# Kernel optimization log

Measured on AMD Instinct MI355X. Metric: run time of the kernel, lower is better.

## Reference

```python
import jax, jax.numpy as jnp
import numpy as np

B, F, T, C = 2, 4, 1024, 1536   # batch, features, ticks, channels
NW = [476, 476, 292]            # wires per plane (same layout for both faces)
NX = 1536                       # wire crossings per face


def _make_wc(rng, nw, nchan):
    # rows: (wire_ident, channel); idents form a permutation of [0, nw)
    ident = rng.permutation(nw)
    chan = rng.integers(0, nchan, size=nw)
    return jnp.asarray(np.stack([ident, chan], axis=1), dtype=jnp.int32)


def setup_inputs() -> dict:
    key = jax.random.key(0)
    rng = np.random.default_rng(0)
    x = jax.random.normal(key, (B, F, T, C), dtype=jnp.float32)
    wcs = {f"wc{i}{j}": _make_wc(rng, NW[j], C) for i in range(2) for j in range(3)}
    xms = {f"xm{i}": jnp.asarray(
        np.stack([rng.integers(0, NW[j], size=NX) for j in range(3)], axis=1),
        dtype=jnp.int32) for i in range(2)}
    w_seg = jax.random.normal(jax.random.fold_in(key, 1), (1, F), dtype=jnp.float32) * 0.1
    b_seg = jnp.zeros((1,), dtype=jnp.float32)
    return {"x": x, **wcs, **xms, "w_seg": w_seg, "b_seg": b_seg}


def _face(x, wcs_face, xm):
    # x: (B,F,T,C); wcs_face: list of 3 (nw,2) int maps; xm: (NX,3)
    outs = []
    for j in range(3):
        ident, chan = wcs_face[j][:, 0], wcs_face[j][:, 1]
        nw = wcs_face[j].shape[0]
        # gather channels, reindex into wire order (scatter-set by wire ident)
        wsv = jnp.zeros(x.shape[:-1] + (nw,), x.dtype).at[..., ident].set(x[..., chan])
        idx = xm[:, j]                                  # (NX,)
        gathered = wsv[..., idx]                        # (B,F,T,NX); crossover term == identity
        # segment-mean back onto wires: scatter_add + count + clamp(min=1)
        summed = jnp.zeros_like(wsv).at[..., idx].add(gathered)
        cnt = jnp.zeros((nw,), x.dtype).at[idx].add(1.0)
        summed = summed / jnp.clip(cnt, 1.0, None)
        outs.append((summed, chan))
    return outs


def reference(x, wc00, wc01, wc02, wc10, wc11, wc12, xm0, xm1, w_seg, b_seg):
    wcs = [[wc00, wc01, wc02], [wc10, wc11, wc12]]
    xms = [xm0, xm1]
    nchan = x.shape[-1]
    y = jnp.zeros_like(x)                # (B,F,T,C)
    cy = jnp.zeros((nchan,), x.dtype)
    for i in range(2):
        for summed, chan in _face(x, wcs[i], xms[i]):
            y = y.at[..., chan].add(summed)   # scatter-add wire terms onto channels
            cy = cy.at[chan].add(1.0)
    y = y / jnp.clip(cy, 1.0, None)
    y = jnp.transpose(y, (0, 1, 3, 2))        # (B,F,C,T)
    logits = jnp.einsum('bfct,of->boct', y, w_seg) + b_seg[None, :, None, None]
    return jax.nn.sigmoid(logits)             # (B,1,C,T)
```

## Files before the change

### kernel.cpp

```cpp
#include <hip/hip_runtime.h>

#define B_ 2
#define F_ 4
#define T_ 1024
#define C_ 1536
#define NX_ 1536
#define CAP 64

__global__ __launch_bounds__(1024) void build_meta(
    const int* __restrict__ wc00, const int* __restrict__ wc01, const int* __restrict__ wc02,
    const int* __restrict__ wc10, const int* __restrict__ wc11, const int* __restrict__ wc12,
    const int* __restrict__ xm0, const int* __restrict__ xm1,
    int nw0, int nw1, int nw2,
    int* __restrict__ masks,
    int* __restrict__ cyInt,
    int* __restrict__ count,
    int* __restrict__ edges,
    float* __restrict__ scale)
{
    const int tid = threadIdx.x;
    const int nth = blockDim.x;
    const int* wcs[6] = {wc00, wc01, wc02, wc10, wc11, wc12};
    const int* xms[2] = {xm0, xm1};
    int nws[3] = {nw0, nw1, nw2};
    int moff[6];
    int tot = 0;
    for (int f = 0; f < 6; ++f) { moff[f] = tot; tot += nws[f % 3]; }

    for (int s = tid; s < tot; s += nth) masks[s] = 0;
    for (int c = tid; c < C_; c += nth) { cyInt[c] = 0; count[c] = 0; }
    __syncthreads();

    for (int i = 0; i < 2; ++i)
        for (int j = 0; j < 3; ++j) {
            const int f = i * 3 + j;
            const int* xm = xms[i];
            for (int p = tid; p < NX_; p += nth) {
                int s = xm[p * 3 + j];
                masks[moff[f] + s] = 1;
            }
        }
    for (int f = 0; f < 6; ++f) {
        const int nw = nws[f % 3];
        const int* wc = wcs[f];
        for (int s = tid; s < nw; s += nth) atomicAdd(&cyInt[wc[s * 2 + 1]], 1);
    }
    __syncthreads();

    for (int f = 0; f < 6; ++f) {
        const int nw = nws[f % 3];
        const int* wc = wcs[f];
        for (int k = tid; k < nw; k += nth) {
            int s = wc[k * 2 + 0];
            if (masks[moff[f] + s]) {
                int dst = wc[s * 2 + 1];
                int src = wc[k * 2 + 1];
                int pos = atomicAdd(&count[dst], 1);
                if (pos < CAP) edges[dst * CAP + pos] = src;
            }
        }
    }
    __syncthreads();

    for (int c = tid; c < C_; c += nth) {
        int cv = cyInt[c];
        scale[c] = 1.0f / (float)(cv > 0 ? cv : 1);
    }
}

#define TILE 64
__global__ __launch_bounds__(256) void zT_kernel(
    const float* __restrict__ x, const float* __restrict__ w_seg,
    float* __restrict__ zT)
{
    __shared__ float tile[TILE][TILE + 1];
    const int b  = blockIdx.z;
    const int t0 = blockIdx.x * TILE;
    const int c0 = blockIdx.y * TILE;
    const int tx = threadIdx.x & 63;
    const int ty = threadIdx.x >> 6;

    const float w0 = w_seg[0], w1 = w_seg[1], w2 = w_seg[2], w3 = w_seg[3];
    const float* xb = x + (size_t)b * F_ * T_ * C_;
    const size_t fstride = (size_t)T_ * C_;

    for (int tt = ty; tt < TILE; tt += 4) {
        const size_t base = (size_t)(t0 + tt) * C_ + c0 + tx;
        float acc = w0 * xb[base]
                  + w1 * xb[base + fstride]
                  + w2 * xb[base + 2 * fstride]
                  + w3 * xb[base + 3 * fstride];
        tile[tt][tx] = acc;
    }
    __syncthreads();

    float* zb = zT + (size_t)b * C_ * T_;
    for (int cc = ty; cc < TILE; cc += 4) {
        zb[(size_t)(c0 + cc) * T_ + t0 + tx] = tile[tx][cc];
    }
}

__global__ __launch_bounds__(256) void gather_out(
    const float* __restrict__ zT,
    const int* __restrict__ edges, const int* __restrict__ count,
    const float* __restrict__ scale, const float* __restrict__ b_seg,
    float* __restrict__ out)
{
    const int c = blockIdx.x;
    const int b = blockIdx.y;
    const int n = min(count[c], CAP);
    const float sc = scale[c];
    const float bs = b_seg[0];

    const float* zb = zT + (size_t)b * C_ * T_;
    const int t = threadIdx.x * 4;

    float4 acc = make_float4(0.f, 0.f, 0.f, 0.f);
    for (int e = 0; e < n; ++e) {
        const int src = edges[c * CAP + e];
        const float4 v = *reinterpret_cast<const float4*>(zb + (size_t)src * T_ + t);
        acc.x += v.x; acc.y += v.y; acc.z += v.z; acc.w += v.w;
    }
    float4 o;
    o.x = 1.f / (1.f + expf(-(acc.x * sc + bs)));
    o.y = 1.f / (1.f + expf(-(acc.y * sc + bs)));
    o.z = 1.f / (1.f + expf(-(acc.z * sc + bs)));
    o.w = 1.f / (1.f + expf(-(acc.w * sc + bs)));
    *reinterpret_cast<float4*>(out + ((size_t)b * C_ + c) * T_ + t) = o;
}

extern "C" void kernel_launch(void* const* d_in, const int* in_sizes, int n_in,
                              void* d_out, int out_size, void* d_ws, size_t ws_size,
                              hipStream_t stream) {
    const float* x     = (const float*)d_in[0];
    const int* wc00    = (const int*)d_in[1];
    const int* wc01    = (const int*)d_in[2];
    const int* wc02    = (const int*)d_in[3];
    const int* wc10    = (const int*)d_in[4];
    const int* wc11    = (const int*)d_in[5];
    const int* wc12    = (const int*)d_in[6];
    const int* xm0     = (const int*)d_in[7];
    const int* xm1     = (const int*)d_in[8];
    const float* w_seg = (const float*)d_in[9];
    const float* b_seg = (const float*)d_in[10];
    float* out         = (float*)d_out;

    const int nw0 = in_sizes[1] / 2;
    const int nw1 = in_sizes[2] / 2;
    const int nw2 = in_sizes[3] / 2;

    char* ws = (char*)d_ws;
    size_t off = 0;
    float* zT   = (float*)(ws + off); off += (size_t)B_ * C_ * T_ * sizeof(float);
    int* edges  = (int*)(ws + off);   off += (size_t)C_ * CAP * sizeof(int);
    int* count  = (int*)(ws + off);   off += (size_t)C_ * sizeof(int);
    int* cyInt  = (int*)(ws + off);   off += (size_t)C_ * sizeof(int);
    float* scale= (float*)(ws + off); off += (size_t)C_ * sizeof(float);
    int* masks  = (int*)(ws + off);   off += (size_t)2 * (nw0 + nw1 + nw2) * sizeof(int);

    build_meta<<<1, 1024, 0, stream>>>(wc00, wc01, wc02, wc10, wc11, wc12,
                                       xm0, xm1, nw0, nw1, nw2,
                                       masks, cyInt, count, edges, scale);

    zT_kernel<<<dim3(T_ / TILE, C_ / TILE, B_), 256, 0, stream>>>(x, w_seg, zT);

    gather_out<<<dim3(C_, B_), 256, 0, stream>>>(zT, edges, count, scale, b_seg, out);
}
```

Before: 128.4 us.

## Fuse metadata build into transpose kernel as extra block with shared-memory atomics

Merges the single-block metadata construction into the weighted-transpose kernel as one extra block, so its work overlaps with the transpose instead of running as a separate serial launch. The metadata masks, counts and channel tallies now live in shared memory instead of global memory. The transpose loads and stores are widened to float4. The cost is a larger shared-memory union (about 28KB) per block, which may reduce occupancy of the transpose blocks, and a hardcoded 4096-entry mask array.

Result: faster. 120.7 us (-6.0%).

```diff
diff --git a/kernel.cpp b/kernel.cpp
--- a/kernel.cpp
+++ b/kernel.cpp
@@ -6,97 +6,119 @@
 #define C_ 1536
 #define NX_ 1536
 #define CAP 64
+#define TILE 64
+#define ZT_BLOCKS ((T_ / TILE) * (C_ / TILE) * B_)
 
-__global__ __launch_bounds__(1024) void build_meta(
+struct MetaSh {
+    int masks[4096];
+    int cnt[C_];
+    int cy[C_];
+};
+
+union SharedU {
+    float tile[TILE][TILE + 1];
+    MetaSh m;
+};
+
+__global__ __launch_bounds__(256) void zt_meta(
+    const float* __restrict__ x, const float* __restrict__ w_seg,
+    float* __restrict__ zT,
     const int* __restrict__ wc00, const int* __restrict__ wc01, const int* __restrict__ wc02,
     const int* __restrict__ wc10, const int* __restrict__ wc11, const int* __restrict__ wc12,
     const int* __restrict__ xm0, const int* __restrict__ xm1,
     int nw0, int nw1, int nw2,
-    int* __restrict__ masks,
-    int* __restrict__ cyInt,
     int* __restrict__ count,
     int* __restrict__ edges,
     float* __restrict__ scale)
 {
+    __shared__ SharedU sh;
     const int tid = threadIdx.x;
-    const int nth = blockDim.x;
-    const int* wcs[6] = {wc00, wc01, wc02, wc10, wc11, wc12};
-    const int* xms[2] = {xm0, xm1};
-    int nws[3] = {nw0, nw1, nw2};
-    int moff[6];
-    int tot = 0;
-    for (int f = 0; f < 6; ++f) { moff[f] = tot; tot += nws[f % 3]; }
 
-    for (int s = tid; s < tot; s += nth) masks[s] = 0;
-    for (int c = tid; c < C_; c += nth) { cyInt[c] = 0; count[c] = 0; }
-    __syncthreads();
+    if (blockIdx.x == ZT_BLOCKS) {
+        const int* wcs[6] = {wc00, wc01, wc02, wc10, wc11, wc12};
+        const int* xms[2] = {xm0, xm1};
+        int nws[3] = {nw0, nw1, nw2};
+        int moff[6];
+        int tot = 0;
+        for (int f = 0; f < 6; ++f) { moff[f] = tot; tot += nws[f % 3]; }
 
-    for (int i = 0; i < 2; ++i)
-        for (int j = 0; j < 3; ++j) {
-            const int f = i * 3 + j;
-            const int* xm = xms[i];
-            for (int p = tid; p < NX_; p += nth) {
-                int s = xm[p * 3 + j];
-                masks[moff[f] + s] = 1;
+        for (int s = tid; s < 4096; s += 256) sh.m.masks[s] = 0;
+        for (int c = tid; c < C_; c += 256) { sh.m.cnt[c] = 0; sh.m.cy[c] = 0; }
+        __syncthreads();
+
+        for (int i = 0; i < 2; ++i)
+            for (int j = 0; j < 3; ++j) {
+                const int f = i * 3 + j;
+                const int* xm = xms[i];
+                for (int p = tid; p < NX_; p += 256)
+                    sh.m.masks[moff[f] + xm[p * 3 + j]] = 1;
+            }
+        __syncthreads();
+
+        for (int f = 0; f < 6; ++f) {
+            const int nw = nws[f % 3];
+            const int* wc = wcs[f];
+            for (int k = tid; k < nw; k += 256) {
+                const int src = wc[k * 2 + 1];
+                atomicAdd(&sh.m.cy[src], 1);
+                const int s = wc[k * 2 + 0];
+                if (sh.m.masks[moff[f] + s]) {
+                    const int dst = wc[s * 2 + 1];
+                    const int pos = atomicAdd(&sh.m.cnt[dst], 1);
+                    if (pos < CAP) edges[dst * CAP + pos] = src;
+                }
             }
         }
-    for (int f = 0; f < 6; ++f) {
-        const int nw = nws[f % 3];
-        const int* wc = wcs[f];
-        for (int s = tid; s < nw; s += nth) atomicAdd(&cyInt[wc[s * 2 + 1]], 1);
+        __syncthreads();
+
+        for (int c = tid; c < C_; c += 256) {
+            count[c] = sh.m.cnt[c];
+            const int cv = sh.m.cy[c];
+            scale[c] = 1.0f / (float)(cv > 0 ? cv : 1);
+        }
+        return;
     }
-    __syncthreads();
 
-    for (int f = 0; f < 6; ++f) {
-        const int nw = nws[f % 3];
-        const int* wc = wcs[f];
-        for (int k = tid; k < nw; k += nth) {
-            int s = wc[k * 2 + 0];
-            if (masks[moff[f] + s]) {
-                int dst = wc[s * 2 + 1];
-                int src = wc[k * 2 + 1];
-                int pos = atomicAdd(&count[dst], 1);
-                if (pos < CAP) edges[dst * CAP + pos] = src;
-            }
-        }
-    }
-    __syncthreads();
+    const int bid  = blockIdx.x;
+    const int tpb  = T_ / TILE;
+    const int b    = bid / (tpb * (C_ / TILE));
+    const int rem  = bid % (tpb * (C_ / TILE));
+    const int t0   = (rem % tpb) * TILE;
+    const int c0   = (rem / tpb) * TILE;
 
-    for (int c = tid; c < C_; c += nth) {
-        int cv = cyInt[c];
-        scale[c] = 1.0f / (float)(cv > 0 ? cv : 1);
-    }
-}
-
-#define TILE 64
-__global__ __launch_bounds__(256) void zT_kernel(
-    const float* __restrict__ x, const float* __restrict__ w_seg,
-    float* __restrict__ zT)
-{
-    __shared__ float tile[TILE][TILE + 1];
-    const int b  = blockIdx.z;
-    const int t0 = blockIdx.x * TILE;
-    const int c0 = blockIdx.y * TILE;
-    const int tx = threadIdx.x & 63;
-    const int ty = threadIdx.x >> 6;
+    const int lo = tid & 15;
+    const int hi = tid >> 4;
 
     const float w0 = w_seg[0], w1 = w_seg[1], w2 = w_seg[2], w3 = w_seg[3];
     const float* xb = x + (size_t)b * F_ * T_ * C_;
-    const size_t fstride = (size_t)T_ * C_;
+    const size_t fs = (size_t)T_ * C_;
 
-    for (int tt = ty; tt < TILE; tt += 4) {
-        const size_t base = (size_t)(t0 + tt) * C_ + c0 + tx;
-        float acc = w0 * xb[base]
-                  + w1 * xb[base + fstride]
-                  + w2 * xb[base + 2 * fstride]
-                  + w3 * xb[base + 3 * fstride];
-        tile[tt][tx] = acc;
+    #pragma unroll
+    for (int p = 0; p < 4; ++p) {
+        const int tt = p * 16 + hi;
+        const size_t base = (size_t)(t0 + tt) * C_ + c0 + lo * 4;
+        const float4 a0 = *reinterpret_cast<const float4*>(xb + base);
+        const float4 a1 = *reinterpret_cast<const float4*>(xb + base + fs);
+        const float4 a2 = *reinterpret_cast<const float4*>(xb + base + 2 * fs);
+        const float4 a3 = *reinterpret_cast<const float4*>(xb + base + 3 * fs);
+        sh.tile[tt][lo * 4 + 0] = w0 * a0.x + w1 * a1.x + w2 * a2.x + w3 * a3.x;
+        sh.tile[tt][lo * 4 + 1] = w0 * a0.y + w1 * a1.y + w2 * a2.y + w3 * a3.y;
+        sh.tile[tt][lo * 4 + 2] = w0 * a0.z + w1 * a1.z + w2 * a2.z + w3 * a3.z;
+        sh.tile[tt][lo * 4 + 3] = w0 * a0.w + w1 * a1.w + w2 * a2.w + w3 * a3.w;
     }
     __syncthreads();
 
     float* zb = zT + (size_t)b * C_ * T_;
-    for (int cc = ty; cc < TILE; cc += 4) {
-        zb[(size_t)(c0 + cc) * T_ + t0 + tx] = tile[tx][cc];
+    #pragma unroll
+    for (int p = 0; p < 4; ++p) {
+        const int cr = p * 16 + hi;
+        const int t4 = lo * 4;
+        float4 o;
+        o.x = sh.tile[t4 + 0][cr];
+        o.y = sh.tile[t4 + 1][cr];
+        o.z = sh.tile[t4 + 2][cr];
+        o.w = sh.tile[t4 + 3][cr];
+        *reinterpret_cast<float4*>(zb + (size_t)(c0 + cr) * T_ + t0 + t4) = o;
     }
 }
 
@@ -151,18 +173,16 @@
 
     char* ws = (char*)d_ws;
     size_t off = 0;
-    float* zT   = (float*)(ws + off); off += (size_t)B_ * C_ * T_ * sizeof(float);
-    int* edges  = (int*)(ws + off);   off += (size_t)C_ * CAP * sizeof(int);
-    int* count  = (int*)(ws + off);   off += (size_t)C_ * sizeof(int);
-    int* cyInt  = (int*)(ws + off);   off += (size_t)C_ * sizeof(int);
-    float* scale= (float*)(ws + off); off += (size_t)C_ * sizeof(float);
-    int* masks  = (int*)(ws + off);   off += (size_t)2 * (nw0 + nw1 + nw2) * sizeof(int);
+    float* zT    = (float*)(ws + off); off += (size_t)B_ * C_ * T_ * sizeof(float);
+    int* edges   = (int*)(ws + off);   off += (size_t)C_ * CAP * sizeof(int);
+    int* count   = (int*)(ws + off);   off += (size_t)C_ * sizeof(int);
+    float* scale = (float*)(ws + off); off += (size_t)C_ * sizeof(float);
 
-    build_meta<<<1, 1024, 0, stream>>>(wc00, wc01, wc02, wc10, wc11, wc12,
-                                       xm0, xm1, nw0, nw1, nw2,
-                                       masks, cyInt, count, edges, scale);
-
-    zT_kernel<<<dim3(T_ / TILE, C_ / TILE, B_), 256, 0, stream>>>(x, w_seg, zT);
+    zt_meta<<<ZT_BLOCKS + 1, 256, 0, stream>>>(
+        x, w_seg, zT,
+        wc00, wc01, wc02, wc10, wc11, wc12,
+        xm0, xm1, nw0, nw1, nw2,
+        count, edges, scale);
 
     gather_out<<<dim3(C_, B_), 256, 0, stream>>>(zT, edges, count, scale, b_seg, out);
 }
```
